# Optimization experiments

Hardware: AMD Instinct MI355X
Metric: run time of the kernel (lower is better)

## Reference

```python
import jax, jax.numpy as jnp
import numpy as np


def sparsemax(z, axis=0):
    # Standard sparsemax projection onto the simplex (Martins & Astudillo 2016).
    n = z.shape[axis]
    # shift by max for numerical stability (invariant for sparsemax)
    z = z - jnp.max(z, axis=axis, keepdims=True)
    z_sorted = -jnp.sort(-z, axis=axis)  # descending sort along axis
    z_cumsum = jnp.cumsum(z_sorted, axis=axis)
    k_shape = [1] * z.ndim
    k_shape[axis] = n
    k = jnp.arange(1, n + 1, dtype=z.dtype).reshape(k_shape)
    support = (1.0 + k * z_sorted) > z_cumsum  # in-support mask
    k_sup = jnp.sum(support, axis=axis, keepdims=True)  # support size (int)
    # cumsum value at index k_sup-1 along axis
    cs_k = jnp.take_along_axis(z_cumsum, k_sup - 1, axis=axis)
    tau = (cs_k - 1.0) / k_sup.astype(z.dtype)
    return jnp.maximum(z - tau, 0.0)


def setup_inputs() -> dict:
    key = jax.random.key(0)
    k_x, k_a = jax.random.split(key)
    x = jax.random.normal(k_x, (4096, 8192), dtype=jnp.float32)
    a = jnp.asarray(1.0, dtype=jnp.float32)  # nn.Parameter initialized to 1.0
    return {"x": x, "a": a}


def reference(x, a):
    z = -jnp.exp(a) * x
    return sparsemax(z, axis=0)
```

## Files before the change

kernel.cpp:

```cpp
#include <hip/hip_runtime.h>
#include <math.h>


constexpr int ROWS = 4096;
constexpr int COLS = 8192;
constexpr int CAPC = 64;
constexpr int CPAD = 16;

constexpr int PANA = 16;
constexpr int NPA  = ROWS / PANA;
constexpr int PANC = 8;

typedef float vfloat4 __attribute__((ext_vector_type(4)));

__global__ __launch_bounds__(1024)
void k_pmax(const float* __restrict__ x, float* __restrict__ pminx,
            int* __restrict__ cnt)
{
    const int t = threadIdx.x;
    const int b = blockIdx.x;

    if (t < 128)
        reinterpret_cast<int4*>(cnt)[b * 128 + t] = make_int4(0, 0, 0, 0);

    const long row0 = (long)b * PANA;

    float m[2][4];
#pragma unroll
    for (int ch = 0; ch < 2; ++ch)
#pragma unroll
        for (int j = 0; j < 4; ++j) m[ch][j] = 3.0e38f;

    for (int r = 0; r < PANA; ++r) {
        const long rb = (row0 + r) * COLS;
#pragma unroll
        for (int ch = 0; ch < 2; ++ch) {
            const int col = ch * 4096 + t * 4;
            const float4 v = *reinterpret_cast<const float4*>(x + rb + col);
            m[ch][0] = fminf(m[ch][0], v.x);
            m[ch][1] = fminf(m[ch][1], v.y);
            m[ch][2] = fminf(m[ch][2], v.z);
            m[ch][3] = fminf(m[ch][3], v.w);
        }
    }
#pragma unroll
    for (int ch = 0; ch < 2; ++ch) {
        float4 o = make_float4(m[ch][0], m[ch][1], m[ch][2], m[ch][3]);
        *reinterpret_cast<float4*>(pminx + (long)b * COLS + ch * 4096 + t * 4) = o;
    }
}

__global__ __launch_bounds__(256)
void k_reduce(const float* __restrict__ pminx, const float* __restrict__ a,
              float* __restrict__ thrx)
{
    const int col = blockIdx.x * 256 + threadIdx.x;
    float m = 3.0e38f;
    for (int p = 0; p < NPA; ++p)
        m = fminf(m, pminx[(long)p * COLS + col]);
    const float s = -expf(a[0]);
    thrx[col] = (s * m - 1.000002f) / s;
}

__global__ __launch_bounds__(512, 2)
void k_filterzero(const float* __restrict__ x, const float* __restrict__ a,
                  const float* __restrict__ thrx,
                  int* __restrict__ cnt, float2* __restrict__ cand,
                  float* __restrict__ out)
{
    __shared__ float tl[COLS];
    const int t = threadIdx.x;
    for (int i = t; i < COLS / 4; i += 512)
        reinterpret_cast<float4*>(tl)[i] =
            reinterpret_cast<const float4*>(thrx)[i];
    __syncthreads();

    const long row0 = (long)blockIdx.x * PANC;
    const float s   = -expf(a[0]);
    const vfloat4 z4 = {0.f, 0.f, 0.f, 0.f};

    for (int r = 0; r < PANC; ++r) {
        const int  row = (int)row0 + r;
        const long rb  = (long)row * COLS;
#pragma unroll
        for (int ch = 0; ch < 4; ++ch) {
            const int col = ch * 2048 + t * 4;
            const float4 v  = *reinterpret_cast<const float4*>(x + rb + col);
            const float4 th = *reinterpret_cast<const float4*>(tl + col);
            __builtin_nontemporal_store(z4,
                reinterpret_cast<vfloat4*>(out + rb + col));
            if (v.x < th.x) { int i = atomicAdd(&cnt[(col + 0) * CPAD], 1);
                if (i < CAPC) cand[(long)(col + 0) * CAPC + i] =
                    make_float2(s * v.x, __int_as_float(row)); }
            if (v.y < th.y) { int i = atomicAdd(&cnt[(col + 1) * CPAD], 1);
                if (i < CAPC) cand[(long)(col + 1) * CAPC + i] =
                    make_float2(s * v.y, __int_as_float(row)); }
            if (v.z < th.z) { int i = atomicAdd(&cnt[(col + 2) * CPAD], 1);
                if (i < CAPC) cand[(long)(col + 2) * CAPC + i] =
                    make_float2(s * v.z, __int_as_float(row)); }
            if (v.w < th.w) { int i = atomicAdd(&cnt[(col + 3) * CPAD], 1);
                if (i < CAPC) cand[(long)(col + 3) * CAPC + i] =
                    make_float2(s * v.w, __int_as_float(row)); }
        }
    }
}

__global__ __launch_bounds__(256, 4)
void k_solve(const int* __restrict__ cnt, const float2* __restrict__ cand,
             const float* __restrict__ x, const float* __restrict__ a,
             float* __restrict__ out)
{
    const int lane = threadIdx.x & 63;
    const int col  = blockIdx.x * 4 + (threadIdx.x >> 6);
    const int K    = cnt[col * CPAD];

    if (K <= CAPC) {
        float v = -3.3e38f; int row = 0;
        if (lane < K) {
            const float2 p = cand[(long)col * CAPC + lane];
            v = p.x; row = __float_as_int(p.y);
        }
        float t = -3.0e38f, prev = 0.f;
        for (int it = 0; it < CAPC + 4; ++it) {
            const bool act = v > t;
            float ss = act ? v : 0.f;
            float sc = act ? 1.f : 0.f;
#pragma unroll
            for (int m = 1; m < 64; m <<= 1) {
                ss += __shfl_xor(ss, m, 64);
                sc += __shfl_xor(sc, m, 64);
            }
            t = (ss - 1.0f) / sc;
            if (sc == prev) break;
            prev = sc;
        }
        if (v > t) out[(long)row * COLS + col] = v - t;
    } else {
        const float s = -expf(a[0]);
        float t = -3.0e38f, prev = 0.f;
        for (int it = 0; it < 256; ++it) {
            float ss = 0.f, sc = 0.f;
            for (int i = 0; i < ROWS / 64; ++i) {
                const float zz = s * x[(long)(lane + i * 64) * COLS + col];
                if (zz > t) { ss += zz; sc += 1.f; }
            }
#pragma unroll
            for (int m = 1; m < 64; m <<= 1) {
                ss += __shfl_xor(ss, m, 64);
                sc += __shfl_xor(sc, m, 64);
            }
            t = (ss - 1.0f) / sc;
            if (sc == prev) break;
            prev = sc;
        }
        for (int i = 0; i < ROWS / 64; ++i) {
            const long r = lane + i * 64;
            const float zz = s * x[r * COLS + col];
            if (zz > t) out[r * COLS + col] = zz - t;
        }
    }
}

extern "C" void kernel_launch(void* const* d_in, const int* in_sizes, int n_in,
                              void* d_out, int out_size, void* d_ws, size_t ws_size,
                              hipStream_t stream) {
    const float* x = (const float*)d_in[0];
    const float* a = (const float*)d_in[1];
    float* out = (float*)d_out;

    char*   ws    = (char*)d_ws;
    int*    cnt   = (int*)ws;
    float*  thrx  = (float*)(ws + 512 * 1024);
    float*  pminx = (float*)(ws + 1024 * 1024);
    float2* cand  = (float2*)(ws + 9 * 1024 * 1024);

    hipLaunchKernelGGL(k_pmax,      dim3(NPA),         dim3(1024), 0, stream,
                       x, pminx, cnt);
    hipLaunchKernelGGL(k_reduce,    dim3(COLS / 256),  dim3(256),  0, stream,
                       pminx, a, thrx);
    hipLaunchKernelGGL(k_filterzero,dim3(ROWS / PANC), dim3(512),  0, stream,
                       x, a, thrx, cnt, cand, out);
    hipLaunchKernelGGL(k_solve,     dim3(COLS / 4),    dim3(256),  0, stream,
                       cnt, cand, x, a, out);
}
```

Measured before the change: 289.3 us.

## Fuse sparsemax pipeline into one cooperative kernel with grid syncs

Replaces the four separate launches (partial min, reduce, filter/zero, solve) with one cooperative kernel of 256 blocks of 1024 threads. The phases are separated by grid-wide syncs, and each block keeps the same 16-row slab for both the min pass and the filter pass. Zeroing of the output moves from nontemporal stores inside the filter kernel to a hipMemsetAsync. The aim is to remove launch gaps and possibly get cache reuse of the slab. In exchange it runs only one block per CU, the reduce phase uses just 8 blocks, and grid syncs add cost.

```diff
diff --git a/kernel.cpp b/kernel.cpp
--- a/kernel.cpp
+++ b/kernel.cpp
@@ -1,94 +1,77 @@
 #include <hip/hip_runtime.h>
+#include <hip/hip_cooperative_groups.h>
 #include <math.h>
 
+
+namespace cg = cooperative_groups;
 
 constexpr int ROWS = 4096;
 constexpr int COLS = 8192;
 constexpr int CAPC = 64;
 constexpr int CPAD = 16;
+constexpr int SLAB = 16;
+constexpr int NSLAB = ROWS / SLAB;
 
-constexpr int PANA = 16;
-constexpr int NPA  = ROWS / PANA;
-constexpr int PANC = 8;
+__global__ __launch_bounds__(1024, 1)
+void k_fused(const float* __restrict__ x, const float* __restrict__ a,
+             int* __restrict__ cnt, float* __restrict__ pminx,
+             float* __restrict__ thrx, float2* __restrict__ cand,
+             float* __restrict__ out)
+{
+    cg::grid_group grid = cg::this_grid();
+    __shared__ float tl[COLS];
 
-typedef float vfloat4 __attribute__((ext_vector_type(4)));
-
-__global__ __launch_bounds__(1024)
-void k_pmax(const float* __restrict__ x, float* __restrict__ pminx,
-            int* __restrict__ cnt)
-{
     const int t = threadIdx.x;
     const int b = blockIdx.x;
 
     if (t < 128)
         reinterpret_cast<int4*>(cnt)[b * 128 + t] = make_int4(0, 0, 0, 0);
 
-    const long row0 = (long)b * PANA;
+    const float s   = -expf(a[0]);
+    const long row0 = (long)b * SLAB;
 
-    float m[2][4];
-#pragma unroll
-    for (int ch = 0; ch < 2; ++ch)
-#pragma unroll
-        for (int j = 0; j < 4; ++j) m[ch][j] = 3.0e38f;
+    float m0=3e38f,m1=3e38f,m2=3e38f,m3=3e38f,
+          m4=3e38f,m5=3e38f,m6=3e38f,m7=3e38f;
+    for (int r = 0; r < SLAB; ++r) {
+        const long rb = (row0 + r) * COLS;
+        float4 v = *reinterpret_cast<const float4*>(x + rb + t * 4);
+        m0 = fminf(m0, v.x); m1 = fminf(m1, v.y);
+        m2 = fminf(m2, v.z); m3 = fminf(m3, v.w);
+        v = *reinterpret_cast<const float4*>(x + rb + 4096 + t * 4);
+        m4 = fminf(m4, v.x); m5 = fminf(m5, v.y);
+        m6 = fminf(m6, v.z); m7 = fminf(m7, v.w);
+    }
+    *reinterpret_cast<float4*>(pminx + (long)b * COLS + t * 4) =
+        make_float4(m0, m1, m2, m3);
+    *reinterpret_cast<float4*>(pminx + (long)b * COLS + 4096 + t * 4) =
+        make_float4(m4, m5, m6, m7);
 
-    for (int r = 0; r < PANA; ++r) {
-        const long rb = (row0 + r) * COLS;
+    __threadfence();
+    grid.sync();
+
+    if (b < 8) {
+        const int col = b * 1024 + t;
+        float mm = 3e38f;
+        for (int p = 0; p < NSLAB; ++p)
+            mm = fminf(mm, pminx[(long)p * COLS + col]);
+        thrx[col] = (s * mm - 1.000002f) / s;
+    }
+
+    __threadfence();
+    grid.sync();
+
+    for (int i = t; i < COLS / 4; i += 1024)
+        reinterpret_cast<float4*>(tl)[i] =
+            reinterpret_cast<const float4*>(thrx)[i];
+    __syncthreads();
+    for (int r = 0; r < SLAB; ++r) {
+        const int  row = (int)row0 + r;
+        const long rb  = (long)row * COLS;
 #pragma unroll
         for (int ch = 0; ch < 2; ++ch) {
             const int col = ch * 4096 + t * 4;
-            const float4 v = *reinterpret_cast<const float4*>(x + rb + col);
-            m[ch][0] = fminf(m[ch][0], v.x);
-            m[ch][1] = fminf(m[ch][1], v.y);
-            m[ch][2] = fminf(m[ch][2], v.z);
-            m[ch][3] = fminf(m[ch][3], v.w);
-        }
-    }
-#pragma unroll
-    for (int ch = 0; ch < 2; ++ch) {
-        float4 o = make_float4(m[ch][0], m[ch][1], m[ch][2], m[ch][3]);
-        *reinterpret_cast<float4*>(pminx + (long)b * COLS + ch * 4096 + t * 4) = o;
-    }
-}
-
-__global__ __launch_bounds__(256)
-void k_reduce(const float* __restrict__ pminx, const float* __restrict__ a,
-              float* __restrict__ thrx)
-{
-    const int col = blockIdx.x * 256 + threadIdx.x;
-    float m = 3.0e38f;
-    for (int p = 0; p < NPA; ++p)
-        m = fminf(m, pminx[(long)p * COLS + col]);
-    const float s = -expf(a[0]);
-    thrx[col] = (s * m - 1.000002f) / s;
-}
-
-__global__ __launch_bounds__(512, 2)
-void k_filterzero(const float* __restrict__ x, const float* __restrict__ a,
-                  const float* __restrict__ thrx,
-                  int* __restrict__ cnt, float2* __restrict__ cand,
-                  float* __restrict__ out)
-{
-    __shared__ float tl[COLS];
-    const int t = threadIdx.x;
-    for (int i = t; i < COLS / 4; i += 512)
-        reinterpret_cast<float4*>(tl)[i] =
-            reinterpret_cast<const float4*>(thrx)[i];
-    __syncthreads();
-
-    const long row0 = (long)blockIdx.x * PANC;
-    const float s   = -expf(a[0]);
-    const vfloat4 z4 = {0.f, 0.f, 0.f, 0.f};
-
-    for (int r = 0; r < PANC; ++r) {
-        const int  row = (int)row0 + r;
-        const long rb  = (long)row * COLS;
-#pragma unroll
-        for (int ch = 0; ch < 4; ++ch) {
-            const int col = ch * 2048 + t * 4;
             const float4 v  = *reinterpret_cast<const float4*>(x + rb + col);
             const float4 th = *reinterpret_cast<const float4*>(tl + col);
-            __builtin_nontemporal_store(z4,
-                reinterpret_cast<vfloat4*>(out + rb + col));
             if (v.x < th.x) { int i = atomicAdd(&cnt[(col + 0) * CPAD], 1);
                 if (i < CAPC) cand[(long)(col + 0) * CAPC + i] =
                     make_float2(s * v.x, __int_as_float(row)); }
@@ -103,60 +86,59 @@
                     make_float2(s * v.w, __int_as_float(row)); }
         }
     }
-}
 
-__global__ __launch_bounds__(256, 4)
-void k_solve(const int* __restrict__ cnt, const float2* __restrict__ cand,
-             const float* __restrict__ x, const float* __restrict__ a,
-             float* __restrict__ out)
-{
-    const int lane = threadIdx.x & 63;
-    const int col  = blockIdx.x * 4 + (threadIdx.x >> 6);
-    const int K    = cnt[col * CPAD];
+    __threadfence();
+    grid.sync();
 
-    if (K <= CAPC) {
-        float v = -3.3e38f; int row = 0;
-        if (lane < K) {
-            const float2 p = cand[(long)col * CAPC + lane];
-            v = p.x; row = __float_as_int(p.y);
-        }
-        float t = -3.0e38f, prev = 0.f;
-        for (int it = 0; it < CAPC + 4; ++it) {
-            const bool act = v > t;
-            float ss = act ? v : 0.f;
-            float sc = act ? 1.f : 0.f;
+    const int lane = t & 63;
+    const int W    = (b << 4) | (t >> 6);
 #pragma unroll
-            for (int m = 1; m < 64; m <<= 1) {
-                ss += __shfl_xor(ss, m, 64);
-                sc += __shfl_xor(sc, m, 64);
+    for (int q = 0; q < 2; ++q) {
+        const int col = W * 2 + q;
+        const int K   = cnt[col * CPAD];
+        if (K <= CAPC) {
+            float v = -3.3e38f; int row = 0;
+            if (lane < K) {
+                const float2 p = cand[(long)col * CAPC + lane];
+                v = p.x; row = __float_as_int(p.y);
             }
-            t = (ss - 1.0f) / sc;
-            if (sc == prev) break;
-            prev = sc;
-        }
-        if (v > t) out[(long)row * COLS + col] = v - t;
-    } else {
-        const float s = -expf(a[0]);
-        float t = -3.0e38f, prev = 0.f;
-        for (int it = 0; it < 256; ++it) {
-            float ss = 0.f, sc = 0.f;
+            float tau = -3.0e38f, prev = 0.f;
+            for (int it = 0; it < CAPC + 4; ++it) {
+                const bool act = v > tau;
+                float ss = act ? v : 0.f;
+                float sc = act ? 1.f : 0.f;
+#pragma unroll
+                for (int m = 1; m < 64; m <<= 1) {
+                    ss += __shfl_xor(ss, m, 64);
+                    sc += __shfl_xor(sc, m, 64);
+                }
+                tau = (ss - 1.0f) / sc;
+                if (sc == prev) break;
+                prev = sc;
+            }
+            if (v > tau) out[(long)row * COLS + col] = v - tau;
+        } else {
+            float tau = -3.0e38f, prev = 0.f;
+            for (int it = 0; it < 256; ++it) {
+                float ss = 0.f, sc = 0.f;
+                for (int i = 0; i < ROWS / 64; ++i) {
+                    const float zz = s * x[(long)(lane + i * 64) * COLS + col];
+                    if (zz > tau) { ss += zz; sc += 1.f; }
+                }
+#pragma unroll
+                for (int m = 1; m < 64; m <<= 1) {
+                    ss += __shfl_xor(ss, m, 64);
+                    sc += __shfl_xor(sc, m, 64);
+                }
+                tau = (ss - 1.0f) / sc;
+                if (sc == prev) break;
+                prev = sc;
+            }
             for (int i = 0; i < ROWS / 64; ++i) {
-                const float zz = s * x[(long)(lane + i * 64) * COLS + col];
-                if (zz > t) { ss += zz; sc += 1.f; }
+                const long r = lane + i * 64;
+                const float zz = s * x[r * COLS + col];
+                if (zz > tau) out[r * COLS + col] = zz - tau;
             }
-#pragma unroll
-            for (int m = 1; m < 64; m <<= 1) {
-                ss += __shfl_xor(ss, m, 64);
-                sc += __shfl_xor(sc, m, 64);
-            }
-            t = (ss - 1.0f) / sc;
-            if (sc == prev) break;
-            prev = sc;
-        }
-        for (int i = 0; i < ROWS / 64; ++i) {
-            const long r = lane + i * 64;
-            const float zz = s * x[r * COLS + col];
-            if (zz > t) out[r * COLS + col] = zz - t;
         }
     }
 }
@@ -174,12 +156,10 @@
     float*  pminx = (float*)(ws + 1024 * 1024);
     float2* cand  = (float2*)(ws + 9 * 1024 * 1024);
 
-    hipLaunchKernelGGL(k_pmax,      dim3(NPA),         dim3(1024), 0, stream,
-                       x, pminx, cnt);
-    hipLaunchKernelGGL(k_reduce,    dim3(COLS / 256),  dim3(256),  0, stream,
-                       pminx, a, thrx);
-    hipLaunchKernelGGL(k_filterzero,dim3(ROWS / PANC), dim3(512),  0, stream,
-                       x, a, thrx, cnt, cand, out);
-    hipLaunchKernelGGL(k_solve,     dim3(COLS / 4),    dim3(256),  0, stream,
-                       cnt, cand, x, a, out);
+    hipMemsetAsync(out, 0, (size_t)ROWS * COLS * sizeof(float), stream);
+
+    void* args[] = {(void*)&x, (void*)&a, (void*)&cnt, (void*)&pminx,
+                    (void*)&thrx, (void*)&cand, (void*)&out};
+    hipLaunchCooperativeKernel((const void*)k_fused, dim3(NSLAB), dim3(1024),
+                               args, 0, stream);
 }
```

New measurement: 689.1 us. +138.2%, slower.
